# Kernel tuning notes

Hardware: AMD Instinct MI355X
Metric: run time of the kernel (lower is better)

## Reference

```python
import jax, jax.numpy as jnp
import numpy as np

DIM_RES, DIM_IN, DIM_OUT = 8192, 64, 32
TAU, DT, CHAOS, P_CONN = 10.0, 0.1, 1.5, 0.1


def setup_inputs() -> dict:
    key = jax.random.key(0)
    k_u, k_w, k_mask, k_in, k_fb, k_out, k_r, k_o = jax.random.split(key, 8)
    # sparse recurrent weights, variance 1/(p*N), scaled by chaos factor
    mask = (jax.random.uniform(k_mask, (DIM_RES, DIM_RES)) < P_CONN).astype(jnp.float32)
    W = mask * jax.random.normal(k_w, (DIM_RES, DIM_RES)) * jnp.float32(CHAOS / np.sqrt(P_CONN * DIM_RES))
    W_in = jax.random.normal(k_in, (DIM_RES, DIM_IN)) * jnp.float32(1.0 / np.sqrt(DIM_IN))
    W_fb = jax.random.normal(k_fb, (DIM_RES, DIM_OUT)) * jnp.float32(1.0 / np.sqrt(DIM_OUT))
    W_out = jax.random.normal(k_out, (DIM_OUT, DIM_RES)) * jnp.float32(0.01)
    r = jax.random.normal(k_r, (DIM_RES,))
    out_prev = jax.random.normal(k_o, (DIM_OUT,))
    input_signal = jax.random.normal(k_u, (DIM_IN,))
    return {"input_signal": input_signal, "W": W, "W_in": W_in, "W_fb": W_fb,
            "W_out": W_out, "r": r, "out_prev": out_prev}


def reference(input_signal, W, W_in, W_fb, W_out, r, out_prev):
    # state = W r + W_in u + W_fb y   (noise_scaling = 0)
    state = W @ r + W_in @ input_signal + W_fb @ out_prev  # [dim_reservoir]
    # leaky integration: r += dt * (tanh(state) - r) / tau
    r_new = r + (DT / TAU) * (jnp.tanh(state) - r)
    # readout: y = W_out r
    return W_out @ r_new
```

## Files before the change

### kernel.cpp

```cpp
#include <hip/hip_runtime.h>
#include <hip/hip_bf16.h>

constexpr int NRES = 8192;
constexpr int NIN  = 64;
constexpr int NOUT = 32;
constexpr float DT_OVER_TAU = 0.1f / 10.0f;

typedef float float4v __attribute__((ext_vector_type(4)));

__global__ __launch_bounds__(256) void reservoir_state_kernel(
    const float* __restrict__ W,
    const float* __restrict__ W_in,
    const float* __restrict__ W_fb,
    const float* __restrict__ u,
    const float* __restrict__ r,
    const float* __restrict__ y,
    float* __restrict__ r_new)
{
    const int row = blockIdx.x;
    const int t   = threadIdx.x;
    const float* wrow = W + (size_t)row * NRES;

    float acc = 0.0f;
#pragma unroll
    for (int j = 0; j < 8; ++j) {
        const int c = (j * 256 + t) * 4;
        float4v wv = *reinterpret_cast<const float4v*>(wrow + c);
        float4v rv = *reinterpret_cast<const float4v*>(r + c);
        acc += wv[0] * rv[0] + wv[1] * rv[1] + wv[2] * rv[2] + wv[3] * rv[3];
    }
    if (t < NIN)  acc += W_in[row * NIN + t] * u[t];
    if (t < NOUT) acc += W_fb[row * NOUT + t] * y[t];

#pragma unroll
    for (int off = 32; off > 0; off >>= 1)
        acc += __shfl_down(acc, off, 64);

    __shared__ float partial[4];
    const int wid  = t >> 6;
    const int lane = t & 63;
    if (lane == 0) partial[wid] = acc;
    __syncthreads();

    if (t == 0) {
        float state = partial[0] + partial[1] + partial[2] + partial[3];
        float ri = r[row];
        r_new[row] = ri + DT_OVER_TAU * (tanhf(state) - ri);
    }
}

__global__ __launch_bounds__(256) void readout_kernel(
    const float* __restrict__ W_out,
    const float* __restrict__ r_new,
    float* __restrict__ out)
{
    const int row = blockIdx.x;
    const int t   = threadIdx.x;
    const float* wrow = W_out + (size_t)row * NRES;

    float acc = 0.0f;
#pragma unroll
    for (int j = 0; j < 8; ++j) {
        const int c = (j * 256 + t) * 4;
        float4v wv = *reinterpret_cast<const float4v*>(wrow + c);
        float4v rv = *reinterpret_cast<const float4v*>(r_new + c);
        acc += wv[0] * rv[0] + wv[1] * rv[1] + wv[2] * rv[2] + wv[3] * rv[3];
    }

#pragma unroll
    for (int off = 32; off > 0; off >>= 1)
        acc += __shfl_down(acc, off, 64);

    __shared__ float partial[4];
    const int wid  = t >> 6;
    const int lane = t & 63;
    if (lane == 0) partial[wid] = acc;
    __syncthreads();

    if (t == 0)
        out[row] = partial[0] + partial[1] + partial[2] + partial[3];
}

extern "C" void kernel_launch(void* const* d_in, const int* in_sizes, int n_in,
                              void* d_out, int out_size, void* d_ws, size_t ws_size,
                              hipStream_t stream) {
    const float* u     = (const float*)d_in[0];
    const float* W     = (const float*)d_in[1];
    const float* W_in  = (const float*)d_in[2];
    const float* W_fb  = (const float*)d_in[3];
    const float* W_out = (const float*)d_in[4];
    const float* r     = (const float*)d_in[5];
    const float* y     = (const float*)d_in[6];

    float* r_new = (float*)d_ws;
    float* out   = (float*)d_out;

    reservoir_state_kernel<<<NRES, 256, 0, stream>>>(W, W_in, W_fb, u, r, y, r_new);
    readout_kernel<<<NOUT, 256, 0, stream>>>(W_out, r_new, out);
}
```

Measured before the change: 46.35 us.

## Fuse reservoir update and readout into one wave-per-row kernel with atomics

Merges the state-update and readout kernels into a single kernel. Each wavefront now handles four rows of W, reduces with xor shuffles, applies tanh and leaky integration, and accumulates the W_out contribution directly. Per-block partial outputs are combined through shared memory and atomically added to an output buffer that is zeroed by a memset. This removes the intermediate r_new round trip and the second launch, and drops the cross-wave shared-memory reduction per row. In exchange it adds a memset, float atomics with nondeterministic summation order, and strided W_out reads.

```diff
diff --git a/kernel.cpp b/kernel.cpp
--- a/kernel.cpp
+++ b/kernel.cpp
@@ -1,84 +1,67 @@
 #include <hip/hip_runtime.h>
-#include <hip/hip_bf16.h>
 
 constexpr int NRES = 8192;
 constexpr int NIN  = 64;
 constexpr int NOUT = 32;
 constexpr float DT_OVER_TAU = 0.1f / 10.0f;
 
+constexpr int WAVES_PER_BLOCK = 4;
+constexpr int ROWS_PER_WAVE   = 4;
+constexpr int NBLOCKS = NRES / (WAVES_PER_BLOCK * ROWS_PER_WAVE);
+
 typedef float float4v __attribute__((ext_vector_type(4)));
 
-__global__ __launch_bounds__(256) void reservoir_state_kernel(
+__global__ __launch_bounds__(256) void reservoir_fused_kernel(
     const float* __restrict__ W,
     const float* __restrict__ W_in,
     const float* __restrict__ W_fb,
+    const float* __restrict__ W_out,
     const float* __restrict__ u,
     const float* __restrict__ r,
-    const float* __restrict__ y,
-    float* __restrict__ r_new)
+    const float* __restrict__ yprev,
+    float* __restrict__ out)
 {
-    const int row = blockIdx.x;
-    const int t   = threadIdx.x;
-    const float* wrow = W + (size_t)row * NRES;
+    const int t     = threadIdx.x;
+    const int wave  = t >> 6;
+    const int lane  = t & 63;
+    const int gwave = blockIdx.x * WAVES_PER_BLOCK + wave;
 
-    float acc = 0.0f;
-#pragma unroll
-    for (int j = 0; j < 8; ++j) {
-        const int c = (j * 256 + t) * 4;
-        float4v wv = *reinterpret_cast<const float4v*>(wrow + c);
-        float4v rv = *reinterpret_cast<const float4v*>(r + c);
-        acc += wv[0] * rv[0] + wv[1] * rv[1] + wv[2] * rv[2] + wv[3] * rv[3];
-    }
-    if (t < NIN)  acc += W_in[row * NIN + t] * u[t];
-    if (t < NOUT) acc += W_fb[row * NOUT + t] * y[t];
+    float yacc = 0.0f;
+
+    for (int i = 0; i < ROWS_PER_WAVE; ++i) {
+        const int row = gwave * ROWS_PER_WAVE + i;
+        const float* wrow = W + (size_t)row * NRES;
+
+        float acc = 0.0f;
+#pragma unroll 8
+        for (int j = 0; j < NRES / (64 * 4); ++j) {
+            const int c = (j * 64 + lane) * 4;
+            float4v wv = *reinterpret_cast<const float4v*>(wrow + c);
+            float4v rv = *reinterpret_cast<const float4v*>(r + c);
+            acc += wv[0] * rv[0] + wv[1] * rv[1] + wv[2] * rv[2] + wv[3] * rv[3];
+        }
+        acc += W_in[row * NIN + lane] * u[lane];
+        if (lane < NOUT) acc += W_fb[row * NOUT + lane] * yprev[lane];
 
 #pragma unroll
-    for (int off = 32; off > 0; off >>= 1)
-        acc += __shfl_down(acc, off, 64);
+        for (int m = 32; m > 0; m >>= 1)
+            acc += __shfl_xor(acc, m, 64);
 
-    __shared__ float partial[4];
-    const int wid  = t >> 6;
-    const int lane = t & 63;
-    if (lane == 0) partial[wid] = acc;
+        const float ri   = r[row];
+        const float rnew = ri + DT_OVER_TAU * (tanhf(acc) - ri);
+
+        if (lane < NOUT)
+            yacc += W_out[(size_t)lane * NRES + row] * rnew;
+    }
+
+    __shared__ float ybuf[WAVES_PER_BLOCK][NOUT];
+    if (lane < NOUT) ybuf[wave][lane] = yacc;
     __syncthreads();
 
-    if (t == 0) {
-        float state = partial[0] + partial[1] + partial[2] + partial[3];
-        float ri = r[row];
-        r_new[row] = ri + DT_OVER_TAU * (tanhf(state) - ri);
+    if (wave == 0 && lane < NOUT) {
+        float s = ybuf[0][lane] + ybuf[1][lane] + ybuf[2][lane] + ybuf[3][lane];
+        atomicAdd(&out[lane], s);
     }
-}
-
-__global__ __launch_bounds__(256) void readout_kernel(
-    const float* __restrict__ W_out,
-    const float* __restrict__ r_new,
-    float* __restrict__ out)
-{
-    const int row = blockIdx.x;
-    const int t   = threadIdx.x;
-    const float* wrow = W_out + (size_t)row * NRES;
-
-    float acc = 0.0f;
-#pragma unroll
-    for (int j = 0; j < 8; ++j) {
-        const int c = (j * 256 + t) * 4;
-        float4v wv = *reinterpret_cast<const float4v*>(wrow + c);
-        float4v rv = *reinterpret_cast<const float4v*>(r_new + c);
-        acc += wv[0] * rv[0] + wv[1] * rv[1] + wv[2] * rv[2] + wv[3] * rv[3];
-    }
-
-#pragma unroll
-    for (int off = 32; off > 0; off >>= 1)
-        acc += __shfl_down(acc, off, 64);
-
-    __shared__ float partial[4];
-    const int wid  = t >> 6;
-    const int lane = t & 63;
-    if (lane == 0) partial[wid] = acc;
-    __syncthreads();
-
-    if (t == 0)
-        out[row] = partial[0] + partial[1] + partial[2] + partial[3];
 }
 
 extern "C" void kernel_launch(void* const* d_in, const int* in_sizes, int n_in,
@@ -90,11 +73,11 @@
     const float* W_fb  = (const float*)d_in[3];
     const float* W_out = (const float*)d_in[4];
     const float* r     = (const float*)d_in[5];
-    const float* y     = (const float*)d_in[6];
+    const float* yprev = (const float*)d_in[6];
 
-    float* r_new = (float*)d_ws;
-    float* out   = (float*)d_out;
+    float* out = (float*)d_out;
 
-    reservoir_state_kernel<<<NRES, 256, 0, stream>>>(W, W_in, W_fb, u, r, y, r_new);
-    readout_kernel<<<NOUT, 256, 0, stream>>>(W_out, r_new, out);
+    hipMemsetAsync(out, 0, NOUT * sizeof(float), stream);
+    reservoir_fused_kernel<<<NBLOCKS, 256, 0, stream>>>(
+        W, W_in, W_fb, W_out, u, r, yprev, out);
 }
```

Measured after the change: 52.66 us. +13.6%, slower.

## Fuse readout into reservoir kernel via atomic accumulation and nontemporal W loads

Applied to the files above, without the earlier changes.

Removes the separate readout kernel. Each reservoir row block now computes its r_new value and atomically adds its contribution W_out[:,row]*r_new into the 32 outputs, after a memset zeroes them. The large W matrix is also read with nontemporal loads to reduce cache pollution. In exchange, each launch issues 8192*32 float atomics to 32 addresses, reads W_out with a strided, uncoalesced pattern, and makes the summation order nondeterministic.

```diff
diff --git a/kernel.cpp b/kernel.cpp
--- a/kernel.cpp
+++ b/kernel.cpp
@@ -1,5 +1,4 @@
 #include <hip/hip_runtime.h>
-#include <hip/hip_bf16.h>
 
 constexpr int NRES = 8192;
 constexpr int NIN  = 64;
@@ -8,14 +7,15 @@
 
 typedef float float4v __attribute__((ext_vector_type(4)));
 
-__global__ __launch_bounds__(256) void reservoir_state_kernel(
+__global__ __launch_bounds__(256) void reservoir_fused_kernel(
     const float* __restrict__ W,
     const float* __restrict__ W_in,
     const float* __restrict__ W_fb,
+    const float* __restrict__ W_out,
     const float* __restrict__ u,
     const float* __restrict__ r,
-    const float* __restrict__ y,
-    float* __restrict__ r_new)
+    const float* __restrict__ yprev,
+    float* __restrict__ out)
 {
     const int row = blockIdx.x;
     const int t   = threadIdx.x;
@@ -25,18 +25,20 @@
 #pragma unroll
     for (int j = 0; j < 8; ++j) {
         const int c = (j * 256 + t) * 4;
-        float4v wv = *reinterpret_cast<const float4v*>(wrow + c);
+        float4v wv = __builtin_nontemporal_load(
+                         reinterpret_cast<const float4v*>(wrow + c));
         float4v rv = *reinterpret_cast<const float4v*>(r + c);
         acc += wv[0] * rv[0] + wv[1] * rv[1] + wv[2] * rv[2] + wv[3] * rv[3];
     }
     if (t < NIN)  acc += W_in[row * NIN + t] * u[t];
-    if (t < NOUT) acc += W_fb[row * NOUT + t] * y[t];
+    if (t < NOUT) acc += W_fb[row * NOUT + t] * yprev[t];
 
 #pragma unroll
     for (int off = 32; off > 0; off >>= 1)
         acc += __shfl_down(acc, off, 64);
 
     __shared__ float partial[4];
+    __shared__ float srnew;
     const int wid  = t >> 6;
     const int lane = t & 63;
     if (lane == 0) partial[wid] = acc;
@@ -45,40 +47,12 @@
     if (t == 0) {
         float state = partial[0] + partial[1] + partial[2] + partial[3];
         float ri = r[row];
-        r_new[row] = ri + DT_OVER_TAU * (tanhf(state) - ri);
+        srnew = ri + DT_OVER_TAU * (tanhf(state) - ri);
     }
-}
-
-__global__ __launch_bounds__(256) void readout_kernel(
-    const float* __restrict__ W_out,
-    const float* __restrict__ r_new,
-    float* __restrict__ out)
-{
-    const int row = blockIdx.x;
-    const int t   = threadIdx.x;
-    const float* wrow = W_out + (size_t)row * NRES;
-
-    float acc = 0.0f;
-#pragma unroll
-    for (int j = 0; j < 8; ++j) {
-        const int c = (j * 256 + t) * 4;
-        float4v wv = *reinterpret_cast<const float4v*>(wrow + c);
-        float4v rv = *reinterpret_cast<const float4v*>(r_new + c);
-        acc += wv[0] * rv[0] + wv[1] * rv[1] + wv[2] * rv[2] + wv[3] * rv[3];
-    }
-
-#pragma unroll
-    for (int off = 32; off > 0; off >>= 1)
-        acc += __shfl_down(acc, off, 64);
-
-    __shared__ float partial[4];
-    const int wid  = t >> 6;
-    const int lane = t & 63;
-    if (lane == 0) partial[wid] = acc;
     __syncthreads();
 
-    if (t == 0)
-        out[row] = partial[0] + partial[1] + partial[2] + partial[3];
+    if (t < NOUT)
+        atomicAdd(&out[t], W_out[(size_t)t * NRES + row] * srnew);
 }
 
 extern "C" void kernel_launch(void* const* d_in, const int* in_sizes, int n_in,
@@ -90,11 +64,11 @@
     const float* W_fb  = (const float*)d_in[3];
     const float* W_out = (const float*)d_in[4];
     const float* r     = (const float*)d_in[5];
-    const float* y     = (const float*)d_in[6];
+    const float* yprev = (const float*)d_in[6];
 
-    float* r_new = (float*)d_ws;
-    float* out   = (float*)d_out;
+    float* out = (float*)d_out;
 
-    reservoir_state_kernel<<<NRES, 256, 0, stream>>>(W, W_in, W_fb, u, r, y, r_new);
-    readout_kernel<<<NOUT, 256, 0, stream>>>(W_out, r_new, out);
+    hipMemsetAsync(out, 0, NOUT * sizeof(float), stream);
+    reservoir_fused_kernel<<<NRES, 256, 0, stream>>>(
+        W, W_in, W_fb, W_out, u, r, yprev, out);
 }
```

Result: slower. 126.0 us (+171.8%).
